# Kernel tuning notes

Hardware: AMD Instinct MI355X
Metric: run time of the kernel (lower is better)

Reference implementation:

```python
import jax, jax.numpy as jnp
import numpy as np

T, B, NIN, NH = 4096, 512, 42, 9  # seq_len, batch, input_size, hidden_size


def setup_inputs() -> dict:
    key = jax.random.key(0)
    k1, k2, k3, k4, k5, k6, k7 = jax.random.split(key, 7)
    bound = 1.0 / np.sqrt(NH)  # PyTorch LSTM init: U(-1/sqrt(hidden), 1/sqrt(hidden))
    return {
        "x": jax.random.normal(k1, (T, B, NIN), dtype=jnp.float32),
        "h": jax.random.normal(k2, (1, B, NH), dtype=jnp.float32),
        "c": jax.random.normal(k3, (1, B, NH), dtype=jnp.float32),
        "W_ih": jax.random.uniform(k4, (4 * NH, NIN), minval=-bound, maxval=bound, dtype=jnp.float32),
        "W_hh": jax.random.uniform(k5, (4 * NH, NH), minval=-bound, maxval=bound, dtype=jnp.float32),
        "b_ih": jax.random.uniform(k6, (4 * NH,), minval=-bound, maxval=bound, dtype=jnp.float32),
        "b_hh": jax.random.uniform(k7, (4 * NH,), minval=-bound, maxval=bound, dtype=jnp.float32),
    }


def _lstm(x, h0, c0, W_ih, W_hh, b_ih, b_hh):
    # Precompute input projection for all timesteps in one GEMM: (T,B,4H)
    x_pre = jnp.einsum('tbi,gi->tbg', x, W_ih) + b_ih

    def step(carry, xt):
        h, c = carry  # (B,H) each
        gates = xt + h @ W_hh.T + b_hh  # (B,4H), PyTorch gate order i,f,g,o
        i, f, g, o = jnp.split(gates, 4, axis=-1)
        i = jax.nn.sigmoid(i)
        f = jax.nn.sigmoid(f)
        g = jnp.tanh(g)
        o = jax.nn.sigmoid(o)
        c_new = f * c + i * g
        h_new = o * jnp.tanh(c_new)
        return (h_new, c_new), h_new

    (hT, cT), outs = jax.lax.scan(step, (h0[0], c0[0]), x_pre)
    return outs, hT[None], cT[None]


def reference(x, h, c, W_ih, W_hh, b_ih, b_hh):
    output, hn, cn = _lstm(x, h, c, W_ih, W_hh, b_ih, b_hh)
    return (output, hn, cn)
```

## Files before the change

### kernel.cpp

```cpp
#include <hip/hip_runtime.h>


#define TT 4096
#define BB 512
#define NIN 42
#define NH 9
#define G4 36
#define PF 8

typedef float v2f __attribute__((ext_vector_type(2)));

__device__ __forceinline__ float fast_sigmoid(float x) {
  float e = __builtin_amdgcn_exp2f(-1.4426950408889634f * x);
  return __builtin_amdgcn_rcpf(1.0f + e);
}
__device__ __forceinline__ float fast_tanh(float x) {
  float e = __builtin_amdgcn_exp2f(2.8853900817779268f * x);
  return 1.0f - 2.0f * __builtin_amdgcn_rcpf(1.0f + e);
}

#define BCAST16(dst, src, k)                                                   \
  dst = __int_as_float(__builtin_amdgcn_ds_swizzle(__float_as_int(src),        \
                                                   ((k) << 5) | 0x10))

__global__ __launch_bounds__(256) void proj_kernel(
    const float* __restrict__ x, const float* __restrict__ W_ih,
    const float* __restrict__ b_ih, const float* __restrict__ b_hh,
    float* __restrict__ P) {
  __shared__ float xs[256 * NIN];
  const int tid = threadIdx.x;
  const size_t rowBase = (size_t)blockIdx.x * 256;

  const float4* xv4 = (const float4*)(x + rowBase * NIN);
  float4* xs4 = (float4*)xs;
#pragma unroll
  for (int it = 0; it < 11; ++it) {
    int idx = tid + it * 256;
    if (idx < 2688) xs4[idx] = xv4[idx];
  }
  __syncthreads();

  float acc[G4];
#pragma unroll
  for (int m = 0; m < G4; m++) {
    int j = m >> 2, g = m & 3;
    acc[m] = b_ih[g * NH + j] + b_hh[g * NH + j];
  }
  const float* xr = xs + tid * NIN;
#pragma unroll
  for (int k = 0; k < NIN; k++) {
    float xk = xr[k];
#pragma unroll
    for (int m = 0; m < G4; m++) {
      int j = m >> 2, g = m & 3;
      acc[m] += xk * W_ih[(g * NH + j) * NIN + k];
    }
  }

  float4* o = (float4*)(P + (rowBase + tid) * (size_t)G4);
#pragma unroll
  for (int q = 0; q < NH; q++)
    o[q] = make_float4(acc[4 * q], acc[4 * q + 1], acc[4 * q + 2], acc[4 * q + 3]);
}

__global__ __launch_bounds__(64) void lstm_kernel(
    const float* __restrict__ P, const float* __restrict__ h0,
    const float* __restrict__ c0, const float* __restrict__ W_hh,
    float* __restrict__ out) {
  const int lane = threadIdx.x;
  const int cl = lane >> 4;
  const int j = lane & 15;
  const bool act = (j < NH);
  const int jj = act ? j : 0;
  const int b = blockIdx.x * 4 + cl;

  v2f Wif[NH], Wgo[NH];
#pragma unroll
  for (int k = 0; k < NH; k++) {
    Wif[k] = (v2f){W_hh[(0 * NH + jj) * NH + k], W_hh[(1 * NH + jj) * NH + k]};
    Wgo[k] = (v2f){W_hh[(2 * NH + jj) * NH + k], W_hh[(3 * NH + jj) * NH + k]};
  }

  float h = h0[b * NH + jj];
  float c = c0[b * NH + jj];

  const float4* Pv = (const float4*)P;
  const size_t stride = (size_t)BB * NH;
  const size_t base = (size_t)b * NH + jj;

  float4 pre[PF];
#pragma unroll
  for (int i = 0; i < PF; i++) pre[i] = Pv[(size_t)i * stride + base];

  for (int t0 = 0; t0 < TT; t0 += PF) {
#pragma unroll
    for (int u = 0; u < PF; u++) {
      const int t = t0 + u;
      float4 p = pre[u];
      float h0r, h1r, h2r, h3r, h4r, h5r, h6r, h7r, h8r;
      BCAST16(h0r, h, 0); BCAST16(h1r, h, 1); BCAST16(h2r, h, 2);
      BCAST16(h3r, h, 3); BCAST16(h4r, h, 4); BCAST16(h5r, h, 5);
      BCAST16(h6r, h, 6); BCAST16(h7r, h, 7); BCAST16(h8r, h, 8);

      v2f a0 = (v2f){p.x, p.y} + Wif[0] * h0r;
      v2f a1 = Wif[1] * h1r;
      v2f a2 = Wif[2] * h2r;
      a0 += Wif[3] * h3r; a1 += Wif[4] * h4r; a2 += Wif[5] * h5r;
      a0 += Wif[6] * h6r; a1 += Wif[7] * h7r; a2 += Wif[8] * h8r;
      v2f gif = (a0 + a1) + a2;

      v2f d0 = (v2f){p.z, p.w} + Wgo[0] * h0r;
      v2f d1 = Wgo[1] * h1r;
      v2f d2 = Wgo[2] * h2r;
      d0 += Wgo[3] * h3r; d1 += Wgo[4] * h4r; d2 += Wgo[5] * h5r;
      d0 += Wgo[6] * h6r; d1 += Wgo[7] * h7r; d2 += Wgo[8] * h8r;
      v2f ggo = (d0 + d1) + d2;

      float i_ = fast_sigmoid(gif.x);
      float f_ = fast_sigmoid(gif.y);
      float g_ = fast_tanh(ggo.x);
      float o_ = fast_sigmoid(ggo.y);
      c = f_ * c + i_ * g_;
      h = o_ * fast_tanh(c);
      if (act) out[(size_t)t * stride + base] = h;

      int tn = t + PF;
      if (tn > TT - 1) tn = TT - 1;
      pre[u] = Pv[(size_t)tn * stride + base];
    }
  }

  if (act) {
    out[(size_t)TT * stride + (size_t)b * NH + j] = h;
    out[(size_t)TT * stride + stride + (size_t)b * NH + j] = c;
  }
}

extern "C" void kernel_launch(void* const* d_in, const int* in_sizes, int n_in,
                              void* d_out, int out_size, void* d_ws, size_t ws_size,
                              hipStream_t stream) {
  (void)in_sizes; (void)n_in; (void)out_size; (void)ws_size;
  const float* x    = (const float*)d_in[0];
  const float* h0   = (const float*)d_in[1];
  const float* c0   = (const float*)d_in[2];
  const float* W_ih = (const float*)d_in[3];
  const float* W_hh = (const float*)d_in[4];
  const float* b_ih = (const float*)d_in[5];
  const float* b_hh = (const float*)d_in[6];
  float* out = (float*)d_out;
  float* P   = (float*)d_ws;

  proj_kernel<<<(TT * BB) / 256, 256, 0, stream>>>(x, W_ih, b_ih, b_hh, P);
  lstm_kernel<<<BB / 4, 64, 0, stream>>>(P, h0, c0, W_hh, out);
}
```

Baseline: 1.354 ms.

## Replace ds_swizzle broadcasts with DPP row rotations and stage W_ih in LDS

```diff
diff --git a/kernel.cpp b/kernel.cpp
--- a/kernel.cpp
+++ b/kernel.cpp
@@ -19,17 +19,25 @@
   return 1.0f - 2.0f * __builtin_amdgcn_rcpf(1.0f + e);
 }
 
-#define BCAST16(dst, src, k)                                                   \
-  dst = __int_as_float(__builtin_amdgcn_ds_swizzle(__float_as_int(src),        \
-                                                   ((k) << 5) | 0x10))
+#define ROR16(dst, src, S)                                                     \
+  dst = __int_as_float(__builtin_amdgcn_update_dpp(                            \
+      0, __float_as_int(src), 0x120 + (S), 0xF, 0xF, true))
 
 __global__ __launch_bounds__(256) void proj_kernel(
     const float* __restrict__ x, const float* __restrict__ W_ih,
     const float* __restrict__ b_ih, const float* __restrict__ b_hh,
     float* __restrict__ P) {
   __shared__ float xs[256 * NIN];
+  __shared__ float ws[NIN * G4];
   const int tid = threadIdx.x;
   const size_t rowBase = (size_t)blockIdx.x * 256;
+
+  for (int idx = tid; idx < NIN * G4; idx += 256) {
+    int k = idx / G4;
+    int m = idx - k * G4;
+    int j = m >> 2, g = m & 3;
+    ws[idx] = W_ih[(g * NH + j) * NIN + k];
+  }
 
   const float4* xv4 = (const float4*)(x + rowBase * NIN);
   float4* xs4 = (float4*)xs;
@@ -46,14 +54,23 @@
     int j = m >> 2, g = m & 3;
     acc[m] = b_ih[g * NH + j] + b_hh[g * NH + j];
   }
+
   const float* xr = xs + tid * NIN;
+  float xv[NIN];
+#pragma unroll
+  for (int k = 0; k < NIN; k++) xv[k] = xr[k];
+
 #pragma unroll
   for (int k = 0; k < NIN; k++) {
-    float xk = xr[k];
+    float xk = xv[k];
+    const float4* wv = (const float4*)(ws + k * G4);
 #pragma unroll
-    for (int m = 0; m < G4; m++) {
-      int j = m >> 2, g = m & 3;
-      acc[m] += xk * W_ih[(g * NH + j) * NIN + k];
+    for (int q = 0; q < NH; q++) {
+      float4 w = wv[q];
+      acc[4 * q + 0] += xk * w.x;
+      acc[4 * q + 1] += xk * w.y;
+      acc[4 * q + 2] += xk * w.z;
+      acc[4 * q + 3] += xk * w.w;
     }
   }
 
@@ -74,11 +91,16 @@
   const int jj = act ? j : 0;
   const int b = blockIdx.x * 4 + cl;
 
-  v2f Wif[NH], Wgo[NH];
+  v2f Wif[16], Wgo[16];
 #pragma unroll
-  for (int k = 0; k < NH; k++) {
-    Wif[k] = (v2f){W_hh[(0 * NH + jj) * NH + k], W_hh[(1 * NH + jj) * NH + k]};
-    Wgo[k] = (v2f){W_hh[(2 * NH + jj) * NH + k], W_hh[(3 * NH + jj) * NH + k]};
+  for (int s = 0; s < 16; s++) {
+    int k = (j - s) & 15;
+    int kk = (k < NH) ? k : 0;
+    float vm = (act && k < NH) ? 1.f : 0.f;
+    Wif[s] = (v2f){vm * W_hh[(0 * NH + jj) * NH + kk],
+                   vm * W_hh[(1 * NH + jj) * NH + kk]};
+    Wgo[s] = (v2f){vm * W_hh[(2 * NH + jj) * NH + kk],
+                   vm * W_hh[(3 * NH + jj) * NH + kk]};
   }
 
   float h = h0[b * NH + jj];
@@ -97,24 +119,31 @@
     for (int u = 0; u < PF; u++) {
       const int t = t0 + u;
       float4 p = pre[u];
-      float h0r, h1r, h2r, h3r, h4r, h5r, h6r, h7r, h8r;
-      BCAST16(h0r, h, 0); BCAST16(h1r, h, 1); BCAST16(h2r, h, 2);
-      BCAST16(h3r, h, 3); BCAST16(h4r, h, 4); BCAST16(h5r, h, 5);
-      BCAST16(h6r, h, 6); BCAST16(h7r, h, 7); BCAST16(h8r, h, 8);
 
-      v2f a0 = (v2f){p.x, p.y} + Wif[0] * h0r;
-      v2f a1 = Wif[1] * h1r;
-      v2f a2 = Wif[2] * h2r;
-      a0 += Wif[3] * h3r; a1 += Wif[4] * h4r; a2 += Wif[5] * h5r;
-      a0 += Wif[6] * h6r; a1 += Wif[7] * h7r; a2 += Wif[8] * h8r;
-      v2f gif = (a0 + a1) + a2;
+      float r1, r2, r3, r4, r5, r6, r7, r8, r9, r10, r11, r12, r13, r14, r15;
+      ROR16(r1, h, 1);   ROR16(r2, h, 2);   ROR16(r3, h, 3);
+      ROR16(r4, h, 4);   ROR16(r5, h, 5);   ROR16(r6, h, 6);
+      ROR16(r7, h, 7);   ROR16(r8, h, 8);   ROR16(r9, h, 9);
+      ROR16(r10, h, 10); ROR16(r11, h, 11); ROR16(r12, h, 12);
+      ROR16(r13, h, 13); ROR16(r14, h, 14); ROR16(r15, h, 15);
 
-      v2f d0 = (v2f){p.z, p.w} + Wgo[0] * h0r;
-      v2f d1 = Wgo[1] * h1r;
-      v2f d2 = Wgo[2] * h2r;
-      d0 += Wgo[3] * h3r; d1 += Wgo[4] * h4r; d2 += Wgo[5] * h5r;
-      d0 += Wgo[6] * h6r; d1 += Wgo[7] * h7r; d2 += Wgo[8] * h8r;
-      v2f ggo = (d0 + d1) + d2;
+      v2f a0 = (v2f){p.x, p.y} + Wif[0] * h;
+      v2f a1 = Wif[1] * r1;
+      v2f a2 = Wif[2] * r2;
+      v2f a3 = Wif[3] * r3;
+      a0 += Wif[4] * r4;   a1 += Wif[5] * r5;   a2 += Wif[6] * r6;   a3 += Wif[7] * r7;
+      a0 += Wif[8] * r8;   a1 += Wif[9] * r9;   a2 += Wif[10] * r10; a3 += Wif[11] * r11;
+      a0 += Wif[12] * r12; a1 += Wif[13] * r13; a2 += Wif[14] * r14; a3 += Wif[15] * r15;
+      v2f gif = (a0 + a1) + (a2 + a3);
+
+      v2f d0 = (v2f){p.z, p.w} + Wgo[0] * h;
+      v2f d1 = Wgo[1] * r1;
+      v2f d2 = Wgo[2] * r2;
+      v2f d3 = Wgo[3] * r3;
+      d0 += Wgo[4] * r4;   d1 += Wgo[5] * r5;   d2 += Wgo[6] * r6;   d3 += Wgo[7] * r7;
+      d0 += Wgo[8] * r8;   d1 += Wgo[9] * r9;   d2 += Wgo[10] * r10; d3 += Wgo[11] * r11;
+      d0 += Wgo[12] * r12; d1 += Wgo[13] * r13; d2 += Wgo[14] * r14; d3 += Wgo[15] * r15;
+      v2f ggo = (d0 + d1) + (d2 + d3);
 
       float i_ = fast_sigmoid(gif.x);
       float f_ = fast_sigmoid(gif.y);
```

After: 1.570 ms. 15.9% more time.
